# Kernel tuning notes

Hardware: AMD Instinct MI355X
Metric: run time of the kernel (lower is better)

Reference implementation:

```python
import jax, jax.numpy as jnp
import numpy as np

N = 100000
E = 1600000
NEG_SLOPE_ATTN = 0.2   # DGL GATConv default negative_slope
NEG_SLOPE_ACT = 0.01   # F.leaky_relu default


def gat_conv(x, src, dst, W, al, ar, b):
    """DGL-style GATConv with a single head.
    x: [N, Fin]; W: [Fin, H*Fout]; al, ar: [H, Fout]; b: [H*Fout].
    Returns [N, H, Fout]."""
    H, Fout = al.shape
    h = (x @ W).reshape(-1, H, Fout)                 # [N,H,Fout]
    el = jnp.sum(h * al, axis=-1)                    # [N,H]
    er = jnp.sum(h * ar, axis=-1)                    # [N,H]
    e = jax.nn.leaky_relu(el[src] + er[dst], NEG_SLOPE_ATTN)  # [E,H]
    # edge softmax over incoming edges of each dst node
    m = jax.ops.segment_max(e, dst, num_segments=N)  # [N,H]
    ex = jnp.exp(e - m[dst])                         # [E,H]
    denom = jax.ops.segment_sum(ex, dst, num_segments=N)      # [N,H]
    a = ex / denom[dst]                              # [E,H]
    msg = h[src] * a[:, :, None]                     # [E,H,Fout]
    out = jax.ops.segment_sum(msg, dst, num_segments=N)       # [N,H,Fout]
    return out + b.reshape(1, H, Fout)


def setup_inputs() -> dict:
    key = jax.random.key(0)
    ks = jax.random.split(key, 16)
    features = jax.random.normal(ks[0], (N, 3), dtype=jnp.float32)
    src = jax.random.randint(ks[1], (E,), 0, N)
    dst = jax.random.randint(ks[2], (E,), 0, N)

    def glorot(k, shape):
        fan = shape[0] + shape[-1]
        s = jnp.sqrt(2.0 / fan).astype(jnp.float32)
        return jax.random.normal(k, shape, dtype=jnp.float32) * s

    W1 = glorot(ks[3], (3, 64));   al1 = glorot(ks[4], (1, 64));  ar1 = glorot(ks[5], (1, 64));  b1 = jnp.zeros((64,), jnp.float32)
    W2 = glorot(ks[6], (64, 64));  al2 = glorot(ks[7], (1, 64));  ar2 = glorot(ks[8], (1, 64));  b2 = jnp.zeros((64,), jnp.float32)
    W3 = glorot(ks[9], (64, 3));   al3 = glorot(ks[10], (1, 3));  ar3 = glorot(ks[11], (1, 3));  b3 = jnp.zeros((3,), jnp.float32)
    return {"features": features, "src": src, "dst": dst,
            "W1": W1, "al1": al1, "ar1": ar1, "b1": b1,
            "W2": W2, "al2": al2, "ar2": ar2, "b2": b2,
            "W3": W3, "al3": al3, "ar3": ar3, "b3": b3}


def reference(features, src, dst, W1, al1, ar1, b1, W2, al2, ar2, b2, W3, al3, ar3, b3):
    x = gat_conv(features, src, dst, W1, al1, ar1, b1)      # [N,1,64]
    x = jax.nn.leaky_relu(x, NEG_SLOPE_ACT)
    x = gat_conv(x[:, 0, :], src, dst, W2, al2, ar2, b2)     # [N,1,64]
    x = jax.nn.leaky_relu(x, NEG_SLOPE_ACT)
    x = gat_conv(x[:, 0, :], src, dst, W3, al3, ar3, b3)     # [N,1,3]
    return x[:, 0, :]                                        # [N,3]
```

## Files before the change

### kernel.cpp

```cpp
#include <hip/hip_runtime.h>
#include <hip/hip_fp16.h>
#include <math.h>


#define NEG_BIG (-1e30f)
#define SORT_CAP 6144
#define BSTRIDE 6144
#define CHUNK 8192

__device__ inline float waveSum(float v) {
#pragma unroll
  for (int off = 32; off; off >>= 1) v += __shfl_xor(v, off, 64);
  return v;
}

__device__ inline float halfSum(float v) {
#pragma unroll
  for (int off = 16; off; off >>= 1) v += __shfl_xor(v, off, 64);
  return v;
}

__device__ inline float halfMax(float v) {
#pragma unroll
  for (int off = 16; off; off >>= 1) v = fmaxf(v, __shfl_xor(v, off, 64));
  return v;
}

__device__ inline int waveMaxI(int v) {
#pragma unroll
  for (int off = 32; off; off >>= 1) v = max(v, __shfl_xor(v, off, 64));
  return v;
}

__device__ inline int rlI(int v, int l) { return __builtin_amdgcn_readlane(v, l); }
__device__ inline float rlF(float v, int l) {
  return __int_as_float(__builtin_amdgcn_readlane(__float_as_int(v), l));
}
__device__ inline int ntI(const int* p) { return __builtin_nontemporal_load(p); }

__global__ __launch_bounds__(1024) void k_bin(
    const int* __restrict__ src, const int* __restrict__ dst,
    int* __restrict__ gcursor, unsigned* __restrict__ binned, int E, int NBK) {
  __shared__ int lcnt[512];
  __shared__ int lbase[512];
  int tid = threadIdx.x;
  for (int b = tid; b < NBK; b += 1024) lcnt[b] = 0;
  __syncthreads();
  int e0 = blockIdx.x * CHUNK;
  int e1 = min(e0 + CHUNK, E);
  for (int e = e0 + tid; e < e1; e += 1024)
    atomicAdd(&lcnt[ntI(&dst[e]) >> 8], 1);
  __syncthreads();
  for (int b = tid; b < NBK; b += 1024) {
    int c = lcnt[b];
    lbase[b] = c ? atomicAdd(&gcursor[b], c) : 0;
    lcnt[b] = 0;
  }
  __syncthreads();
  for (int e = e0 + tid; e < e1; e += 1024) {
    int dd = ntI(&dst[e]);
    int ss = ntI(&src[e]);
    int b = dd >> 8;
    int pos = lbase[b] + atomicAdd(&lcnt[b], 1);
    if (pos < BSTRIDE)
      binned[(size_t)b * BSTRIDE + pos] =
          ((unsigned)(dd & 255) << 24) | (unsigned)ss;
  }
}

__global__ void k_bscan(const int* __restrict__ cnt, int* __restrict__ base,
                        int NBK, int E, int* __restrict__ startv, int N) {
  __shared__ int s[1024];
  int t = threadIdx.x;
  int v = (t < NBK) ? cnt[t] : 0;
  s[t] = v;
  __syncthreads();
  for (int off = 1; off < 1024; off <<= 1) {
    int u = (t >= off) ? s[t - off] : 0;
    __syncthreads();
    s[t] += u;
    __syncthreads();
  }
  int excl = s[t] - v;
  if (t <= NBK) base[t] = excl;
  if (t == 0) startv[N] = E;
}

__global__ __launch_bounds__(256) void k_sort(
    const unsigned* __restrict__ binned, const int* __restrict__ base,
    int* __restrict__ csr, int* __restrict__ startv, int N) {
  __shared__ unsigned sbuf[SORT_CAP];
  __shared__ unsigned obuf[SORT_CAP];
  __shared__ int hist[256];
  __shared__ int scn[256];
  __shared__ int cur[256];
  int b = blockIdx.x;
  int tid = threadIdx.x;
  int gbase = base[b];
  int cnt = min(base[b + 1] - gbase, BSTRIDE);
  const unsigned* bsrc = binned + (size_t)b * BSTRIDE;
  hist[tid] = 0;
  __syncthreads();
  if (cnt <= SORT_CAP) {
    for (int i = tid; i < cnt; i += 256) {
      unsigned w = bsrc[i];
      sbuf[i] = w;
      atomicAdd(&hist[w >> 24], 1);
    }
    __syncthreads();
    int v = hist[tid];
    scn[tid] = v;
    __syncthreads();
    for (int off = 1; off < 256; off <<= 1) {
      int u = (tid >= off) ? scn[tid - off] : 0;
      __syncthreads();
      scn[tid] += u;
      __syncthreads();
    }
    int excl = scn[tid] - v;
    cur[tid] = excl;
    int dn = b * 256 + tid;
    if (dn < N) startv[dn] = gbase + excl;
    __syncthreads();
    for (int i = tid; i < cnt; i += 256) {
      unsigned w = sbuf[i];
      int p = atomicAdd(&cur[w >> 24], 1);
      obuf[p] = w & 0xFFFFFFu;
    }
    __syncthreads();
    for (int i = tid; i < cnt; i += 256) csr[gbase + i] = (int)obuf[i];
  } else {
    for (int i = tid; i < cnt; i += 256)
      atomicAdd(&hist[bsrc[i] >> 24], 1);
    __syncthreads();
    int v = hist[tid];
    scn[tid] = v;
    __syncthreads();
    for (int off = 1; off < 256; off <<= 1) {
      int u = (tid >= off) ? scn[tid - off] : 0;
      __syncthreads();
      scn[tid] += u;
      __syncthreads();
    }
    int excl = scn[tid] - v;
    cur[tid] = excl;
    int dn = b * 256 + tid;
    if (dn < N) startv[dn] = gbase + excl;
    __syncthreads();
    for (int i = tid; i < cnt; i += 256) {
      unsigned w = bsrc[i];
      int p = atomicAdd(&cur[w >> 24], 1);
      csr[gbase + p] = (int)(w & 0xFFFFFFu);
    }
  }
}

__global__ void k_prep(const float* __restrict__ W1, const float* __restrict__ al1,
                       const float* __restrict__ ar1, const float* __restrict__ W2,
                       const float* __restrict__ al2, const float* __restrict__ ar2,
                       float* __restrict__ uvw) {
  int lane = threadIdx.x & 63;
  float a = al1[lane], r = ar1[lane];
#pragma unroll
  for (int i = 0; i < 3; ++i) {
    float w = W1[i * 64 + lane];
    float ui = waveSum(w * a);
    float vi = waveSum(w * r);
    if (lane == 0) { uvw[i] = ui; uvw[3 + i] = vi; }
  }
  float sa = 0.f, sr = 0.f;
  for (int j = 0; j < 64; ++j) {
    float w = W2[lane * 64 + j];
    sa = fmaf(w, al2[j], sa);
    sr = fmaf(w, ar2[j], sr);
  }
  uvw[8 + lane] = sa;
  uvw[72 + lane] = sr;
}

__global__ void k_padx(const float* __restrict__ x, const float* __restrict__ uvw,
                       float4* __restrict__ x4, float* __restrict__ er1, int N) {
  int n = blockIdx.x * blockDim.x + threadIdx.x;
  if (n >= N) return;
  float x0 = __builtin_nontemporal_load(&x[n * 3]);
  float x1 = __builtin_nontemporal_load(&x[n * 3 + 1]);
  float x2 = __builtin_nontemporal_load(&x[n * 3 + 2]);
  float el = fmaf(x0, uvw[0], fmaf(x1, uvw[1], x2 * uvw[2]));
  float er = fmaf(x0, uvw[3], fmaf(x1, uvw[4], x2 * uvw[5]));
  x4[n] = make_float4(x0, x1, x2, el);
  er1[n] = er;
}

__global__ __launch_bounds__(128) void k_agg1x(
    const float4* __restrict__ x4, const float* __restrict__ er1,
    const float* __restrict__ W1, const float* __restrict__ b1,
    const float* __restrict__ uvw, const int* __restrict__ start,
    const int* __restrict__ csr, float4* __restrict__ a4,
    float* __restrict__ er2, int N) {
  __shared__ float4 sWp[64];
  __shared__ float2 sLR[64];
  int tid = threadIdx.x;
  if (tid < 64) {
    sWp[tid] = make_float4(W1[tid], W1[64 + tid], W1[128 + tid], b1[tid]);
    sLR[tid] = make_float2(uvw[8 + tid], uvw[72 + tid]);
  }
  __syncthreads();
  int n = blockIdx.x * 128 + tid;
  if (n >= N) return;
  int beg = start[n], end = start[n + 1];
  float ern = er1[n];
  float m = NEG_BIG, d = 0.f, X0 = 0.f, X1 = 0.f, X2 = 0.f;
  int s0, s1, s2, s3;
  float4 h0, h1, h2, h3v;
  s0 = (beg + 0 < end) ? ntI(&csr[beg + 0]) : 0;
  s0 = ((unsigned)s0 < (unsigned)N) ? s0 : 0; h0 = x4[s0];
  s1 = (beg + 1 < end) ? ntI(&csr[beg + 1]) : 0;
  s1 = ((unsigned)s1 < (unsigned)N) ? s1 : 0; h1 = x4[s1];
  s2 = (beg + 2 < end) ? ntI(&csr[beg + 2]) : 0;
  s2 = ((unsigned)s2 < (unsigned)N) ? s2 : 0; h2 = x4[s2];
  s3 = (beg + 3 < end) ? ntI(&csr[beg + 3]) : 0;
  s3 = ((unsigned)s3 < (unsigned)N) ? s3 : 0; h3v = x4[s3];
  for (int i = beg; i < end; ++i) {
    float4 hv = h0;
    h0 = h1; h1 = h2; h2 = h3v;
    int ip = i + 4;
    int sp = (ip < end) ? ntI(&csr[ip]) : 0;
    sp = ((unsigned)sp < (unsigned)N) ? sp : 0;
    h3v = x4[sp];
    float e = hv.w + ern;
    e = e > 0.f ? e : 0.2f * e;
    float mn = fmaxf(m, e);
    float sc = __expf(m - mn);
    float q = __expf(e - mn);
    d = fmaf(d, sc, q);
    X0 = fmaf(X0, sc, q * hv.x);
    X1 = fmaf(X1, sc, q * hv.y);
    X2 = fmaf(X2, sc, q * hv.z);
    m = mn;
  }
  float inv = (end > beg) ? 1.f / d : 0.f;
  float A0 = X0 * inv, A1 = X1 * inv, A2 = X2 * inv;
  float el = 0.f, er = 0.f;
#pragma unroll 4
  for (int k = 0; k < 64; ++k) {
    float4 w = sWp[k];
    float v = fmaf(A2, w.z, fmaf(A1, w.y, fmaf(A0, w.x, w.w)));
    v = v > 0.f ? v : 0.01f * v;
    float2 lr = sLR[k];
    el = fmaf(v, lr.x, el);
    er = fmaf(v, lr.y, er);
  }
  a4[n] = make_float4(A0, A1, A2, el);
  er2[n] = er;
}

__global__ __launch_bounds__(64) void k_agg2r(
    const float4* __restrict__ a4, const float* __restrict__ er2,
    const int* __restrict__ start, const int* __restrict__ csr,
    const float* __restrict__ W1, const float* __restrict__ b1,
    __half* __restrict__ xa, int N) {
  __shared__ float4 sAV[64];
  int tid = threadIdx.x;
  int lane = tid & 63, hl = lane & 31, half = lane >> 5;
  int pn = blockIdx.x * 2 + half;
  int n = (pn < N) ? pn : 0;
  int beg = start[n], end = start[n + 1];
  int deg = end - beg;
  int maxd = __builtin_amdgcn_readfirstlane(waveMaxI(deg));
  float ern = er2[n];
  int k0 = 2 * hl;
  float wa0 = W1[k0],     wb0 = W1[64 + k0],     wc0 = W1[128 + k0],     bb0 = b1[k0];
  float wa1 = W1[k0 + 1], wb1 = W1[64 + k0 + 1], wc1 = W1[128 + k0 + 1], bb1 = b1[k0 + 1];
  float acc0 = 0.f, acc1 = 0.f;

  float aA = 0.f, v0s = 0.f, v1s = 0.f, v2s = 0.f;
  if (maxd <= 32) {
    int idx = beg + hl;
    int s = (idx < end) ? ntI(&csr[idx]) : 0;
    s = ((unsigned)s < (unsigned)N) ? s : 0;
    float4 av = a4[s];
    float e = av.w + ern;
    e = e > 0.f ? e : 0.2f * e;
    e = (idx < end) ? e : NEG_BIG;
    float mm = halfMax(e);
    float q = __expf(e - mm);
    float dsum = halfSum(q);
    float inv = (deg > 0) ? 1.f / dsum : 0.f;
    aA = q * inv;
    v0s = av.x; v1s = av.y; v2s = av.z;
  }
  sAV[half * 32 + hl] = make_float4(aA, v0s, v1s, v2s);
  __syncthreads();

  if (maxd <= 32) {
    const float4* sp = &sAV[half * 32];
    for (int j = 0; j < maxd; j += 4) {
#pragma unroll
      for (int k = 0; k < 4; ++k) {
        float4 w = sp[j + k];
        float a = w.x;
        float v0 = fmaf(w.w, wc0, fmaf(w.z, wb0, fmaf(w.y, wa0, bb0)));
        v0 = v0 > 0.f ? v0 : 0.01f * v0;
        float v1 = fmaf(w.w, wc1, fmaf(w.z, wb1, fmaf(w.y, wa1, bb1)));
        v1 = v1 > 0.f ? v1 : 0.01f * v1;
        acc0 = fmaf(a, v0, acc0);
        acc1 = fmaf(a, v1, acc1);
      }
    }
  } else {
    float m = NEG_BIG, dsum = 0.f;
    for (int base = beg; base < end; base += 32) {
      int idx = base + hl;
      int s = (idx < end) ? csr[idx] : 0;
      s = ((unsigned)s < (unsigned)N) ? s : 0;
      float e = a4[s].w + ern;
      e = e > 0.f ? e : 0.2f * e;
      e = (idx < end) ? e : NEG_BIG;
      float mn = fmaxf(m, halfMax(e));
      dsum = dsum * __expf(m - mn) + halfSum(__expf(e - mn));
      m = mn;
    }
    float inv = (deg > 0) ? 1.f / dsum : 0.f;
    for (int base = beg; base < end; base += 32) {
      int idx = base + hl;
      int s = (idx < end) ? csr[idx] : 0;
      s = ((unsigned)s < (unsigned)N) ? s : 0;
      float e = a4[s].w + ern;
      e = e > 0.f ? e : 0.2f * e;
      float a = (idx < end) ? __expf(e - m) * inv : 0.f;
      for (int j = 0; j < 32; ++j) {
        int sAx = rlI(s, j), sBx = rlI(s, j + 32);
        float aAx = rlF(a, j), aBx = rlF(a, j + 32);
        int sj = half ? sBx : sAx;
        float aj = half ? aBx : aAx;
        float4 av = a4[sj];
        float v0 = fmaf(av.z, wc0, fmaf(av.y, wb0, fmaf(av.x, wa0, bb0)));
        v0 = v0 > 0.f ? v0 : 0.01f * v0;
        float v1 = fmaf(av.z, wc1, fmaf(av.y, wb1, fmaf(av.x, wa1, bb1)));
        v1 = v1 > 0.f ? v1 : 0.01f * v1;
        acc0 = fmaf(aj, v0, acc0);
        acc1 = fmaf(aj, v1, acc1);
      }
    }
  }
  if (pn < N) {
    __half2 hv = __float22half2_rn(make_float2(acc0, acc1));
    ((__half2*)xa)[(size_t)pn * 32 + hl] = hv;
  }
}

__global__ __launch_bounds__(256) void k_gemm3(
    const __half* xa_in, const float* __restrict__ W2,
    const float* __restrict__ b2, const float* __restrict__ W3,
    const float* __restrict__ al3, float* __restrict__ h3, int N) {
  __shared__ float sW[64 * 64];
  __shared__ float sX[64 * 64];
  __shared__ float sW3[192];
  int tid = threadIdx.x;
  for (int i = tid; i < 4096; i += 256) sW[i] = W2[i];
  if (tid < 192) sW3[tid] = W3[tid];
  const unsigned* xu = (const unsigned*)xa_in;
  size_t base = (size_t)blockIdx.x * 2048;
  size_t limit = (size_t)N * 32;
  for (int i = tid; i < 2048; i += 256) {
    size_t gi = base + i;
    unsigned u = (gi < limit) ? __builtin_nontemporal_load(&xu[gi]) : 0u;
    __half2 hh = *(__half2*)&u;
    float2 f = __half22float2(hh);
    sX[2 * i] = f.x;
    sX[2 * i + 1] = f.y;
  }
  __syncthreads();
  int wave = tid >> 6, f = tid & 63;
  int r0 = wave * 16;
  float acc[16];
#pragma unroll
  for (int i = 0; i < 16; ++i) acc[i] = 0.f;
  const float2* sX2 = (const float2*)sX;
  for (int k2 = 0; k2 < 32; ++k2) {
    float wv0 = sW[(2 * k2) * 64 + f];
    float wv1 = sW[(2 * k2 + 1) * 64 + f];
#pragma unroll
    for (int i = 0; i < 16; ++i) {
      float2 xv = sX2[(r0 + i) * 32 + k2];
      acc[i] = fmaf(xv.x, wv0, fmaf(xv.y, wv1, acc[i]));
    }
  }
  float bf = b2[f];
  __syncthreads();
#pragma unroll
  for (int i = 0; i < 16; ++i) {
    float r = acc[i] + bf;
    r = r > 0.f ? r : 0.01f * r;
    sX[(r0 + i) * 64 + f] = r;
  }
  __syncthreads();
  int row = tid >> 2, j = tid & 3;
  int j3 = (j < 3) ? j : 0;
  float p = 0.f;
  for (int i = 0; i < 64; ++i) {
    int ff = (row + i) & 63;
    p = fmaf(sX[row * 64 + ff], sW3[ff * 3 + j3], p);
  }
  int lb = (tid & 63) & ~3;
  float q0 = __shfl(p, lb + 0, 64);
  float q1 = __shfl(p, lb + 1, 64);
  float q2 = __shfl(p, lb + 2, 64);
  float val = (j < 3) ? p : fmaf(q0, al3[0], fmaf(q1, al3[1], q2 * al3[2]));
  int grow = blockIdx.x * 64 + row;
  if (grow < N) h3[(size_t)blockIdx.x * 256 + tid] = val;
}

__global__ __launch_bounds__(128) void k_agg3(
    const float4* __restrict__ h3, const int* __restrict__ start,
    const int* __restrict__ csr, const float* __restrict__ ar3,
    const float* __restrict__ b, float* __restrict__ out, int N) {
  int n = blockIdx.x * 128 + threadIdx.x;
  if (n >= N) return;
  int beg = start[n], end = start[n + 1];
  float4 hn = h3[n];
  float ern = fmaf(hn.x, ar3[0], fmaf(hn.y, ar3[1], hn.z * ar3[2]));
  float m = NEG_BIG, d = 0.f, Q0 = 0.f, Q1 = 0.f, Q2 = 0.f;
  int s0, s1, s2, s3;
  float4 h0, h1, h2, h3v;
  s0 = (beg + 0 < end) ? ntI(&csr[beg + 0]) : 0;
  s0 = ((unsigned)s0 < (unsigned)N) ? s0 : 0; h0 = h3[s0];
  s1 = (beg + 1 < end) ? ntI(&csr[beg + 1]) : 0;
  s1 = ((unsigned)s1 < (unsigned)N) ? s1 : 0; h1 = h3[s1];
  s2 = (beg + 2 < end) ? ntI(&csr[beg + 2]) : 0;
  s2 = ((unsigned)s2 < (unsigned)N) ? s2 : 0; h2 = h3[s2];
  s3 = (beg + 3 < end) ? ntI(&csr[beg + 3]) : 0;
  s3 = ((unsigned)s3 < (unsigned)N) ? s3 : 0; h3v = h3[s3];
  for (int i = beg; i < end; ++i) {
    float4 hv = h0;
    h0 = h1; h1 = h2; h2 = h3v;
    int ip = i + 4;
    int sp = (ip < end) ? ntI(&csr[ip]) : 0;
    sp = ((unsigned)sp < (unsigned)N) ? sp : 0;
    h3v = h3[sp];
    float e = hv.w + ern;
    e = e > 0.f ? e : 0.2f * e;
    float mn = fmaxf(m, e);
    float sc = __expf(m - mn);
    float q = __expf(e - mn);
    d = fmaf(d, sc, q);
    Q0 = fmaf(Q0, sc, q * hv.x);
    Q1 = fmaf(Q1, sc, q * hv.y);
    Q2 = fmaf(Q2, sc, q * hv.z);
    m = mn;
  }
  float inv = (end > beg) ? 1.f / d : 0.f;
  out[n * 3 + 0] = fmaf(Q0, inv, b[0]);
  out[n * 3 + 1] = fmaf(Q1, inv, b[1]);
  out[n * 3 + 2] = fmaf(Q2, inv, b[2]);
}

extern "C" void kernel_launch(void* const* d_in, const int* in_sizes, int n_in,
                              void* d_out, int out_size, void* d_ws, size_t ws_size,
                              hipStream_t stream) {
  const int N = in_sizes[0] / 3;
  const int E = in_sizes[1];
  const float* feats = (const float*)d_in[0];
  const int* src = (const int*)d_in[1];
  const int* dst = (const int*)d_in[2];
  const float* W1  = (const float*)d_in[3];
  const float* al1 = (const float*)d_in[4];
  const float* ar1 = (const float*)d_in[5];
  const float* b1  = (const float*)d_in[6];
  const float* W2  = (const float*)d_in[7];
  const float* al2 = (const float*)d_in[8];
  const float* ar2 = (const float*)d_in[9];
  const float* b2  = (const float*)d_in[10];
  const float* W3  = (const float*)d_in[11];
  const float* al3 = (const float*)d_in[12];
  const float* ar3 = (const float*)d_in[13];
  const float* b3  = (const float*)d_in[14];

  const int NBK = (N + 255) >> 8;

  char* ws = (char*)d_ws;
  size_t off = 0;
  auto alloc = [&](size_t bytes) -> void* {
    void* p = ws + off;
    off = (off + bytes + 255) & ~(size_t)255;
    return p;
  };
  int* startv  = (int*)alloc((size_t)(N + 1) * 4);
  int* csr     = (int*)alloc((size_t)E * 4);
  float* er2v  = (float*)alloc((size_t)N * 4);
  float* er1   = (float*)alloc((size_t)N * 4);
  int* gcount  = (int*)alloc((size_t)NBK * 4);
  int* baseb   = (int*)alloc((size_t)(NBK + 1) * 4);
  float* uvw   = (float*)alloc(1024);
  float* h3    = (float*)alloc((size_t)N * 4 * 4);
  float4* x4   = (float4*)alloc((size_t)N * 16);
  float4* a4   = (float4*)alloc((size_t)N * 16);
  __half* xa   = (__half*)alloc((size_t)N * 64 * 2);
  unsigned* binned = (unsigned*)xa;

  const int NB  = (N + 255) / 256;
  const int NB1 = (N + 127) / 128;
  const int NW2 = (N + 1) / 2;
  const int GB  = (N + 63) / 64;
  const int CB  = (E + CHUNK - 1) / CHUNK;

  k_prep<<<1, 64, 0, stream>>>(W1, al1, ar1, W2, al2, ar2, uvw);
  k_padx<<<NB, 256, 0, stream>>>(feats, uvw, x4, er1, N);

  hipMemsetAsync(gcount, 0, (size_t)NBK * 4, stream);
  k_bin<<<CB, 1024, 0, stream>>>(src, dst, gcount, binned, E, NBK);
  k_bscan<<<1, 1024, 0, stream>>>(gcount, baseb, NBK, E, startv, N);
  k_sort<<<NBK, 256, 0, stream>>>(binned, baseb, csr, startv, N);

  k_agg1x<<<NB1, 128, 0, stream>>>(x4, er1, W1, b1, uvw, startv, csr,
                                   a4, er2v, N);
  k_agg2r<<<NW2, 64, 0, stream>>>(a4, er2v, startv, csr, W1, b1, xa, N);
  k_gemm3<<<GB, 256, 0, stream>>>(xa, W2, b2, W3, al3, h3, N);
  k_agg3<<<NB1, 128, 0, stream>>>((const float4*)h3, startv, csr, ar3, b3,
                                  (float*)d_out, N);
}
```

Baseline: 251.2 us.

## Fold prep, memset and bucket scan into neighboring kernels to cut launches

Removes three small serial launches: the weight-prep kernel is folded into k_padx (attention projections recomputed per block) and k_agg1x (W2·al2/ar2 recomputed per block), the gcount memset moves into k_padx block 0, and the single-block bucket scan is replaced by each sort block redundantly scanning all bucket counts in shared memory. The aim is to remove launch and serialization gaps between tiny kernels. The cost is redundant per-block compute. The sort-block scan is limited to 512 buckets, which fits N=100000 (391 buckets).

Result: faster. 240.6 us (-4.2%).

```diff
diff --git a/kernel.cpp b/kernel.cpp
--- a/kernel.cpp
+++ b/kernel.cpp
@@ -68,36 +68,32 @@
   }
 }
 
-__global__ void k_bscan(const int* __restrict__ cnt, int* __restrict__ base,
-                        int NBK, int E, int* __restrict__ startv, int N) {
-  __shared__ int s[1024];
-  int t = threadIdx.x;
-  int v = (t < NBK) ? cnt[t] : 0;
-  s[t] = v;
-  __syncthreads();
-  for (int off = 1; off < 1024; off <<= 1) {
-    int u = (t >= off) ? s[t - off] : 0;
-    __syncthreads();
-    s[t] += u;
-    __syncthreads();
-  }
-  int excl = s[t] - v;
-  if (t <= NBK) base[t] = excl;
-  if (t == 0) startv[N] = E;
-}
-
 __global__ __launch_bounds__(256) void k_sort(
-    const unsigned* __restrict__ binned, const int* __restrict__ base,
-    int* __restrict__ csr, int* __restrict__ startv, int N) {
+    const unsigned* __restrict__ binned, const int* __restrict__ gcount,
+    int* __restrict__ csr, int* __restrict__ startv, int N, int E, int NBK) {
   __shared__ unsigned sbuf[SORT_CAP];
   __shared__ unsigned obuf[SORT_CAP];
   __shared__ int hist[256];
   __shared__ int scn[256];
   __shared__ int cur[256];
+  __shared__ int sscan[512];
   int b = blockIdx.x;
   int tid = threadIdx.x;
-  int gbase = base[b];
-  int cnt = min(base[b + 1] - gbase, BSTRIDE);
+  sscan[tid] = (tid < NBK) ? gcount[tid] : 0;
+  sscan[tid + 256] = (tid + 256 < NBK) ? gcount[tid + 256] : 0;
+  __syncthreads();
+  for (int off = 1; off < 512; off <<= 1) {
+    int u0 = (tid >= off) ? sscan[tid - off] : 0;
+    int u1 = (tid + 256 >= off) ? sscan[tid + 256 - off] : 0;
+    __syncthreads();
+    sscan[tid] += u0;
+    sscan[tid + 256] += u1;
+    __syncthreads();
+  }
+  int cntb = gcount[b];
+  int gbase = sscan[b] - cntb;
+  int cnt = min(cntb, BSTRIDE);
+  if (b == 0 && tid == 0) startv[N] = E;
   const unsigned* bsrc = binned + (size_t)b * BSTRIDE;
   hist[tid] = 0;
   __syncthreads();
@@ -155,38 +151,33 @@
   }
 }
 
-__global__ void k_prep(const float* __restrict__ W1, const float* __restrict__ al1,
-                       const float* __restrict__ ar1, const float* __restrict__ W2,
-                       const float* __restrict__ al2, const float* __restrict__ ar2,
-                       float* __restrict__ uvw) {
-  int lane = threadIdx.x & 63;
-  float a = al1[lane], r = ar1[lane];
-#pragma unroll
-  for (int i = 0; i < 3; ++i) {
-    float w = W1[i * 64 + lane];
-    float ui = waveSum(w * a);
-    float vi = waveSum(w * r);
-    if (lane == 0) { uvw[i] = ui; uvw[3 + i] = vi; }
-  }
-  float sa = 0.f, sr = 0.f;
-  for (int j = 0; j < 64; ++j) {
-    float w = W2[lane * 64 + j];
-    sa = fmaf(w, al2[j], sa);
-    sr = fmaf(w, ar2[j], sr);
-  }
-  uvw[8 + lane] = sa;
-  uvw[72 + lane] = sr;
-}
-
-__global__ void k_padx(const float* __restrict__ x, const float* __restrict__ uvw,
-                       float4* __restrict__ x4, float* __restrict__ er1, int N) {
-  int n = blockIdx.x * blockDim.x + threadIdx.x;
+__global__ __launch_bounds__(256) void k_padx(
+    const float* __restrict__ x, const float* __restrict__ W1,
+    const float* __restrict__ al1, const float* __restrict__ ar1,
+    int* __restrict__ gcount, int NBK,
+    float4* __restrict__ x4, float* __restrict__ er1, int N) {
+  __shared__ float su[6];
+  int tid = threadIdx.x;
+  if (tid < 64) {
+    float a = al1[tid], r = ar1[tid];
+#pragma unroll
+    for (int i = 0; i < 3; ++i) {
+      float w = W1[i * 64 + tid];
+      float ui = waveSum(w * a);
+      float vi = waveSum(w * r);
+      if (tid == 0) { su[i] = ui; su[3 + i] = vi; }
+    }
+  }
+  if (blockIdx.x == 0)
+    for (int b = tid; b < NBK; b += 256) gcount[b] = 0;
+  __syncthreads();
+  int n = blockIdx.x * 256 + tid;
   if (n >= N) return;
   float x0 = __builtin_nontemporal_load(&x[n * 3]);
   float x1 = __builtin_nontemporal_load(&x[n * 3 + 1]);
   float x2 = __builtin_nontemporal_load(&x[n * 3 + 2]);
-  float el = fmaf(x0, uvw[0], fmaf(x1, uvw[1], x2 * uvw[2]));
-  float er = fmaf(x0, uvw[3], fmaf(x1, uvw[4], x2 * uvw[5]));
+  float el = fmaf(x0, su[0], fmaf(x1, su[1], x2 * su[2]));
+  float er = fmaf(x0, su[3], fmaf(x1, su[4], x2 * su[5]));
   x4[n] = make_float4(x0, x1, x2, el);
   er1[n] = er;
 }
@@ -194,7 +185,8 @@
 __global__ __launch_bounds__(128) void k_agg1x(
     const float4* __restrict__ x4, const float* __restrict__ er1,
     const float* __restrict__ W1, const float* __restrict__ b1,
-    const float* __restrict__ uvw, const int* __restrict__ start,
+    const float* __restrict__ W2, const float* __restrict__ al2,
+    const float* __restrict__ ar2, const int* __restrict__ start,
     const int* __restrict__ csr, float4* __restrict__ a4,
     float* __restrict__ er2, int N) {
   __shared__ float4 sWp[64];
@@ -202,7 +194,14 @@
   int tid = threadIdx.x;
   if (tid < 64) {
     sWp[tid] = make_float4(W1[tid], W1[64 + tid], W1[128 + tid], b1[tid]);
-    sLR[tid] = make_float2(uvw[8 + tid], uvw[72 + tid]);
+    float sa = 0.f, sr = 0.f;
+#pragma unroll 8
+    for (int f = 0; f < 64; ++f) {
+      float w = W2[tid * 64 + f];
+      sa = fmaf(w, al2[f], sa);
+      sr = fmaf(w, ar2[f], sr);
+    }
+    sLR[tid] = make_float2(sa, sr);
   }
   __syncthreads();
   int n = blockIdx.x * 128 + tid;
@@ -490,8 +489,6 @@
   float* er2v  = (float*)alloc((size_t)N * 4);
   float* er1   = (float*)alloc((size_t)N * 4);
   int* gcount  = (int*)alloc((size_t)NBK * 4);
-  int* baseb   = (int*)alloc((size_t)(NBK + 1) * 4);
-  float* uvw   = (float*)alloc(1024);
   float* h3    = (float*)alloc((size_t)N * 4 * 4);
   float4* x4   = (float4*)alloc((size_t)N * 16);
   float4* a4   = (float4*)alloc((size_t)N * 16);
@@ -504,16 +501,12 @@
   const int GB  = (N + 63) / 64;
   const int CB  = (E + CHUNK - 1) / CHUNK;
 
-  k_prep<<<1, 64, 0, stream>>>(W1, al1, ar1, W2, al2, ar2, uvw);
-  k_padx<<<NB, 256, 0, stream>>>(feats, uvw, x4, er1, N);
-
-  hipMemsetAsync(gcount, 0, (size_t)NBK * 4, stream);
+  k_padx<<<NB, 256, 0, stream>>>(feats, W1, al1, ar1, gcount, NBK,
+                                 x4, er1, N);
   k_bin<<<CB, 1024, 0, stream>>>(src, dst, gcount, binned, E, NBK);
-  k_bscan<<<1, 1024, 0, stream>>>(gcount, baseb, NBK, E, startv, N);
-  k_sort<<<NBK, 256, 0, stream>>>(binned, baseb, csr, startv, N);
-
-  k_agg1x<<<NB1, 128, 0, stream>>>(x4, er1, W1, b1, uvw, startv, csr,
-                                   a4, er2v, N);
+  k_sort<<<NBK, 256, 0, stream>>>(binned, gcount, csr, startv, N, E, NBK);
+  k_agg1x<<<NB1, 128, 0, stream>>>(x4, er1, W1, b1, W2, al2, ar2,
+                                   startv, csr, a4, er2v, N);
   k_agg2r<<<NW2, 64, 0, stream>>>(a4, er2v, startv, csr, W1, b1, xa, N);
   k_gemm3<<<GB, 256, 0, stream>>>(xa, W2, b2, W3, al3, h3, N);
   k_agg3<<<NB1, 128, 0, stream>>>((const float4*)h3, startv, csr, ar3, b3,
```
